# Optimization experiments

Hardware: AMD Instinct MI355X
Metric: run time of the kernel (lower is better)

## Reference

```python
import jax, jax.numpy as jnp
import numpy as np

KS = 3          # kernel_size
NUM_FA = 16     # number of functional atoms per pixel
TOTAL_BASES = 6 # num_bases * (ks // 2)
BN_EPS = 1e-5


def _conv3x3(x, w, b):
    # NCHW conv, padding=1, stride=1
    y = jax.lax.conv_general_dilated(
        x, w, window_strides=(1, 1), padding=[(1, 1), (1, 1)],
        dimension_numbers=("NCHW", "OIHW", "NCHW"))
    return y + b[None, :, None, None]


def _bn(x, gamma, beta, mean, var):
    scale = gamma / jnp.sqrt(var + BN_EPS)
    return (x - mean[None, :, None, None]) * scale[None, :, None, None] + beta[None, :, None, None]


def setup_inputs() -> dict:
    key = jax.random.key(0)
    ks = jax.random.split(key, 16)
    N, C, H, W = 16, 64, 64, 64
    INTER, BC_DIM, O = 64, TOTAL_BASES * NUM_FA, 128
    f32 = jnp.float32
    return {
        "x": jax.random.normal(ks[0], (N, C, H, W), f32),
        "conv1_w": jax.random.normal(ks[1], (INTER, C, 3, 3), f32) * 0.05,
        "conv1_b": jax.random.normal(ks[2], (INTER,), f32) * 0.05,
        "bn1_gamma": jax.random.uniform(ks[3], (INTER,), f32, 0.5, 1.5),
        "bn1_beta": jax.random.normal(ks[4], (INTER,), f32) * 0.05,
        "bn1_mean": jax.random.normal(ks[5], (INTER,), f32) * 0.05,
        "bn1_var": jax.random.uniform(ks[6], (INTER,), f32, 0.5, 1.5),
        "conv2_w": jax.random.normal(ks[7], (BC_DIM, INTER, 3, 3), f32) * 0.05,
        "conv2_b": jax.random.normal(ks[8], (BC_DIM,), f32) * 0.05,
        "bn2_gamma": jax.random.uniform(ks[9], (BC_DIM,), f32, 0.5, 1.5),
        "bn2_beta": jax.random.normal(ks[10], (BC_DIM,), f32) * 0.05,
        "bn2_mean": jax.random.normal(ks[11], (BC_DIM,), f32) * 0.05,
        "bn2_var": jax.random.uniform(ks[12], (BC_DIM,), f32, 0.5, 1.5),
        "bases": jax.random.normal(ks[13], (TOTAL_BASES, KS * KS), f32),
        "coef": jax.random.normal(ks[14], (O, C * NUM_FA), f32) * 0.02,
    }


def reference(x, conv1_w, conv1_b, bn1_gamma, bn1_beta, bn1_mean, bn1_var,
              conv2_w, conv2_b, bn2_gamma, bn2_beta, bn2_mean, bn2_var,
              bases, coef):
    N, C, H, W = x.shape
    # bases_net: conv3x3 -> BN -> tanh -> conv3x3 -> BN -> tanh
    h = jnp.tanh(_bn(_conv3x3(x, conv1_w, conv1_b), bn1_gamma, bn1_beta, bn1_mean, bn1_var))
    bc = jnp.tanh(_bn(_conv3x3(h, conv2_w, conv2_b), bn2_gamma, bn2_beta, bn2_mean, bn2_var))
    # torch: .transpose(1,-1).view(N,H,W,num_fa,total_bases)  (swaps H/W; H==W)
    bases_coef = jnp.transpose(bc, (0, 3, 2, 1)).reshape(N, H, W, NUM_FA, TOTAL_BASES)
    # atoms: (bases_coef[...,None] * bases).sum(-2).transpose(-1,-2) -> (N,H,W,ks2,num_fa)
    atoms = jnp.einsum("nhwft,tk->nhwkf", bases_coef, bases)
    # unfold(x, ks, padding=1) -> patches (N,H,W,C,ks2), channel-major like torch unfold
    xp = jnp.pad(x, ((0, 0), (0, 0), (1, 1), (1, 1)))
    patches = jnp.stack([xp[:, :, i:i + H, j:j + W] for i in range(KS) for j in range(KS)], axis=2)  # (N,C,9,H,W)
    patches = jnp.transpose(patches, (0, 3, 4, 1, 2))  # (N,H,W,C,9)
    # (x.unsqueeze(-1) * atoms.unsqueeze(-3)).sum(-2) -> (N,H,W,C,num_fa) -> flatten C-major
    bases_out = jnp.einsum("nhwck,nhwkf->nhwcf", patches, atoms).reshape(N, H, W, C * NUM_FA)
    # torch: .transpose(1,-1) -> (N, C*num_fa, W, H), then 1x1 conv with coef
    out = jnp.einsum("nhwd,od->nowh", bases_out, coef)  # (N, O, W, H)
    return out
```

## Files before the change

kernel.cpp:

```cpp
#include <hip/hip_runtime.h>
#include <math.h>
#include <string.h>

#define NBATCH 16

typedef __attribute__((ext_vector_type(8))) short short8;
typedef __attribute__((ext_vector_type(4))) float floatx4;
typedef __fp16 half2v __attribute__((ext_vector_type(2)));
#define MFMA16(a, b, c) __builtin_amdgcn_mfma_f32_16x16x32_bf16(a, b, c, 0, 0, 0)

__device__ __forceinline__ unsigned int cvtpk(float a, float b) {
  unsigned int r;
  asm("v_cvt_pk_bf16_f32 %0, %1, %2" : "=v"(r) : "v"(a), "v"(b));
  return r;
}
__device__ __forceinline__ unsigned short f2bf(float f) {
  return (unsigned short)(cvtpk(f, 0.f) & 0xffffu);
}
__device__ __forceinline__ unsigned int packbf2(float a, float b) {
  return cvtpk(a, b);
}
__device__ __forceinline__ float bflo(unsigned int u) {
  return __uint_as_float(u << 16);
}
__device__ __forceinline__ float bfhi(unsigned int u) {
  return __uint_as_float(u & 0xffff0000u);
}
__device__ __forceinline__ float fast_tanh(float x) {
  float e = __expf(2.f * x);
  return 1.f - 2.f / (e + 1.f);
}

__global__ void prep_weights(const float* __restrict__ w1,
                             const float* __restrict__ w2,
                             const float* __restrict__ coef,
                             unsigned short* __restrict__ w1swz,
                             unsigned short* __restrict__ w2swz,
                             unsigned short* __restrict__ coefswz) {
  int i = blockIdx.x * 256 + threadIdx.x;
  if (i < 131072) {
    int j = i & 7, f = i >> 3;
    int lane = f & 63;
    int u = (f >> 6) & 3;
    int wj = (f >> 8) & 1;
    int kc = (f >> 9) & 1;
    int rd = f >> 10;
    int lm = lane & 15, lq = lane >> 4;
    int oc = wj * 64 + u * 16 + lm;
    int k = rd * 64 + kc * 32 + lq * 8 + j;
    coefswz[i] = f2bf(coef[oc * 1024 + k]);
  }
  if (i < 36864) {
    int j = i & 7, f = i >> 3;
    int lane = f & 63;
    int u = (f >> 6) & 1;
    int wn = (f >> 7) & 1;
    int kc = (f >> 8) & 1;
    int off = f >> 9;
    int lm = lane & 15, lq = lane >> 4;
    int oc = wn * 32 + u * 16 + lm;
    int ic = kc * 32 + lq * 8 + j;
    w1swz[i] = f2bf(w1[(oc * 64 + ic) * 9 + off]);
  }
  if (i < 55296) {
    int j = i & 7, f = i >> 3;
    int lane = f & 63;
    int rem = f >> 6;
    int u = rem % 3;
    int rem2 = rem / 3;
    int wn = rem2 & 1;
    int kc = (rem2 >> 1) & 1;
    int off = rem2 >> 2;
    int lm = lane & 15, lq = lane >> 4;
    int oc = wn * 48 + u * 16 + lm;
    int ic = kc * 32 + lq * 8 + j;
    w2swz[i] = f2bf(w2[(oc * 64 + ic) * 9 + off]);
  }
}

__global__ __launch_bounds__(256) void xb_prep(const float* __restrict__ x,
                                               unsigned short* __restrict__ xb) {
  __shared__ float tile[64][65];
  const int t = threadIdx.x;
  const int y = blockIdx.x, n = blockIdx.y;
  const float* xn = x + (size_t)n * 64 * 4096 + y * 64;
#pragma unroll
  for (int it = 0; it < 16; ++it) {
    int idx = it * 256 + t;
    int c = idx >> 6, xx = idx & 63;
    tile[c][xx] = xn[c * 4096 + xx];
  }
  __syncthreads();
  const int xx = t >> 2, cq = t & 3;
  unsigned short* dst = xb + ((size_t)n * 4096 + y * 64 + xx) * 64;
#pragma unroll
  for (int jj = 0; jj < 2; ++jj) {
    int ch0 = cq * 16 + jj * 8;
    unsigned int p[4];
#pragma unroll
    for (int e = 0; e < 4; ++e)
      p[e] = packbf2(tile[ch0 + e * 2][xx], tile[ch0 + e * 2 + 1][xx]);
    *(uint4*)&dst[ch0] = make_uint4(p[0], p[1], p[2], p[3]);
  }
}

__global__ __launch_bounds__(256) void fused_conv(
    const unsigned short* __restrict__ xb, const unsigned short* __restrict__ w1swz,
    const unsigned short* __restrict__ w2swz, const float* __restrict__ b1,
    const float* __restrict__ g1, const float* __restrict__ be1,
    const float* __restrict__ m1, const float* __restrict__ v1,
    const float* __restrict__ b2, const float* __restrict__ g2,
    const float* __restrict__ be2, const float* __restrict__ m2,
    const float* __restrict__ v2, unsigned short* __restrict__ bcg) {
  __shared__ unsigned short xls[144 * 72];
  __shared__ unsigned short hls[128 * 72];

  const int t = threadIdx.x;
  const int tile = blockIdx.x, n = blockIdx.y;
  const int x0 = (tile & 7) * 8, y0 = (tile >> 3) * 8;

  const unsigned short* xbn = xb + (size_t)n * 4096 * 64;
#pragma unroll
  for (int it = 0; it < 5; ++it) {
    int idx = it * 256 + t;
    if (idx < 1152) {
      int pos = idx >> 3, u4 = idx & 7;
      int xr = pos / 12, xc = pos - xr * 12;
      int gy = y0 - 2 + xr, gx = x0 - 2 + xc;
      uint4 v = {0u, 0u, 0u, 0u};
      if ((unsigned)gy < 64u && (unsigned)gx < 64u)
        v = *(const uint4*)&xbn[((size_t)gy * 64 + gx) * 64 + u4 * 8];
      *(uint4*)&xls[pos * 72 + u4 * 8] = v;
    }
  }
  __syncthreads();

  const int lane = t & 63, w = t >> 6;
  const int wm = w & 1, wn = w >> 1;
  const int lm = lane & 15, lq = lane >> 4;

  int abase[4];
#pragma unroll
  for (int i = 0; i < 4; ++i) {
    int px = (wm + 2 * i) * 16 + lm;
    if (px > 99) px = 99;
    int hr = px / 10, hc = px - hr * 10;
    abase[i] = (hr * 12 + hc) * 72 + lq * 8;
  }
  floatx4 acc[4][2];
#pragma unroll
  for (int i = 0; i < 4; ++i)
#pragma unroll
    for (int u = 0; u < 2; ++u) acc[i][u] = floatx4{0.f, 0.f, 0.f, 0.f};

#pragma unroll
  for (int step = 0; step < 18; ++step) {
    const int off = step >> 1, kc = step & 1;
    const int di = off / 3, dj = off % 3;
    short8 b[2];
#pragma unroll
    for (int u = 0; u < 2; ++u)
      b[u] = *(const short8*)&w1swz[(off * 512 + kc * 256 + wn * 128 + u * 64 +
                                     lane) * 8];
#pragma unroll
    for (int i = 0; i < 4; ++i) {
      short8 a = *(const short8*)&xls[abase[i] + (di * 12 + dj) * 72 + kc * 32];
      acc[i][0] = MFMA16(a, b[0], acc[i][0]);
      acc[i][1] = MFMA16(a, b[1], acc[i][1]);
    }
  }
  {
    float sc[2], sh[2];
#pragma unroll
    for (int u = 0; u < 2; ++u) {
      int oc = wn * 32 + u * 16 + lm;
      sc[u] = g1[oc] * rsqrtf(v1[oc] + 1e-5f);
      sh[u] = (b1[oc] - m1[oc]) * sc[u] + be1[oc];
    }
#pragma unroll
    for (int i = 0; i < 4; ++i) {
      int px0 = (wm + 2 * i) * 16 + lq * 4;
#pragma unroll
      for (int u = 0; u < 2; ++u) {
        int oc = wn * 32 + u * 16 + lm;
#pragma unroll
        for (int r = 0; r < 4; ++r) {
          int px = px0 + r;
          if (px < 100) {
            int hr = px / 10, hc = px - hr * 10;
            int gy = y0 - 1 + hr, gx = x0 - 1 + hc;
            bool valid = ((unsigned)gy < 64u) && ((unsigned)gx < 64u);
            float val = valid ? fast_tanh(acc[i][u][r] * sc[u] + sh[u]) : 0.f;
            hls[px * 72 + oc] = f2bf(val);
          }
        }
      }
    }
  }
  __syncthreads();

  int hbase[2];
#pragma unroll
  for (int s = 0; s < 2; ++s) {
    int opx = (wm + 2 * s) * 16 + lm;
    int yl = opx >> 3, xl = opx & 7;
    hbase[s] = (yl * 10 + xl) * 72 + lq * 8;
  }
  floatx4 acc2[2][3];
#pragma unroll
  for (int s = 0; s < 2; ++s)
#pragma unroll
    for (int u = 0; u < 3; ++u) acc2[s][u] = floatx4{0.f, 0.f, 0.f, 0.f};

#pragma unroll
  for (int step = 0; step < 18; ++step) {
    const int off = step >> 1, kc = step & 1;
    const int di = off / 3, dj = off % 3;
    short8 b[3];
#pragma unroll
    for (int u = 0; u < 3; ++u)
      b[u] = *(const short8*)&w2swz[(off * 768 + kc * 384 + wn * 192 + u * 64 +
                                     lane) * 8];
#pragma unroll
    for (int s = 0; s < 2; ++s) {
      short8 a = *(const short8*)&hls[hbase[s] + (di * 10 + dj) * 72 + kc * 32];
      acc2[s][0] = MFMA16(a, b[0], acc2[s][0]);
      acc2[s][1] = MFMA16(a, b[1], acc2[s][1]);
      acc2[s][2] = MFMA16(a, b[2], acc2[s][2]);
    }
  }
  {
    float sc[3], sh[3];
#pragma unroll
    for (int u = 0; u < 3; ++u) {
      int oc = wn * 48 + u * 16 + lm;
      sc[u] = g2[oc] * rsqrtf(v2[oc] + 1e-5f);
      sh[u] = (b2[oc] - m2[oc]) * sc[u] + be2[oc];
    }
    unsigned short* bcn = bcg + (size_t)n * 4096 * 96;
#pragma unroll
    for (int s = 0; s < 2; ++s) {
      int opx0 = (wm + 2 * s) * 16 + lq * 4;
#pragma unroll
      for (int u = 0; u < 3; ++u) {
        int oc = wn * 48 + u * 16 + lm;
#pragma unroll
        for (int r = 0; r < 4; ++r) {
          int opx = opx0 + r;
          int y = y0 + (opx >> 3), xx = x0 + (opx & 7);
          bcn[((size_t)y * 64 + xx) * 96 + oc] =
              f2bf(fast_tanh(acc2[s][u][r] * sc[u] + sh[u]));
        }
      }
    }
  }
}

__global__ __launch_bounds__(256, 2) void adconv_final(
    const unsigned short* __restrict__ xb, const unsigned short* __restrict__ bc,
    const float* __restrict__ bases, const unsigned short* __restrict__ coefswz,
    float* __restrict__ out) {
  __shared__ unsigned short xs[180 * 72];
  __shared__ unsigned short As[4 * 4096];

  const int t = threadIdx.x;
  const int tile = blockIdx.x, n = blockIdx.y;
  const int q0 = (tile & 3) * 16, p0 = (tile >> 2) * 8;

  float bs[54];
#pragma unroll
  for (int i = 0; i < 54; ++i) bs[i] = bases[i];

  const unsigned short* xbn = xb + (size_t)n * 4096 * 64;
#pragma unroll
  for (int it = 0; it < 6; ++it) {
    int idx = it * 256 + t;
    if (idx < 1440) {
      int pos = idx >> 3, u4 = idx & 7;
      int row = pos / 18, col = pos - row * 18;
      int gp = p0 - 1 + row, gq = q0 - 1 + col;
      uint4 v = {0u, 0u, 0u, 0u};
      if ((unsigned)gp < 64u && (unsigned)gq < 64u)
        v = *(const uint4*)&xbn[((size_t)gp * 64 + gq) * 64 + u4 * 8];
      *(uint4*)&xs[pos * 72 + u4 * 8] = v;
    }
  }

  const int lane = t & 63, w = t >> 6;
  const int lm = lane & 15, lq = lane >> 4;

  const int px_a = t >> 1, fh = t & 1;
  const int qx_a = px_a >> 3, py_a = px_a & 7;
  const int pxl_b = lane >> 1;

  half2v atp[9][4];
  {
    const unsigned short* bp =
        bc + ((size_t)n * 4096 + (q0 + qx_a) * 64 + (p0 + py_a)) * 96 + fh * 48;
    float bcv[48];
#pragma unroll
    for (int m = 0; m < 6; ++m) {
      uint4 v = *(const uint4*)(bp + m * 8);
      unsigned int uu[4] = {v.x, v.y, v.z, v.w};
#pragma unroll
      for (int e = 0; e < 4; ++e) {
        bcv[m * 8 + e * 2] = bflo(uu[e]);
        bcv[m * 8 + e * 2 + 1] = bfhi(uu[e]);
      }
    }
#pragma unroll
    for (int j2 = 0; j2 < 4; ++j2)
#pragma unroll
      for (int k = 0; k < 9; ++k) {
        float s0 = 0.f, s1 = 0.f;
#pragma unroll
        for (int tt = 0; tt < 6; ++tt) {
          s0 = fmaf(bcv[(2 * j2) * 6 + tt], bs[tt * 9 + k], s0);
          s1 = fmaf(bcv[(2 * j2 + 1) * 6 + tt], bs[tt * 9 + k], s1);
        }
        atp[k][j2] = __builtin_amdgcn_cvt_pkrtz(s0, s1);
      }
  }

  int pa[9];
#pragma unroll
  for (int i = 0; i < 3; ++i)
#pragma unroll
    for (int j = 0; j < 3; ++j)
      pa[i * 3 + j] = ((py_a + i) * 18 + qx_a + j) * 72;

  floatx4 acc[2][2][4];
#pragma unroll
  for (int s = 0; s < 2; ++s)
#pragma unroll
    for (int wj = 0; wj < 2; ++wj)
#pragma unroll
      for (int u = 0; u < 4; ++u) acc[s][wj][u] = floatx4{0.f, 0.f, 0.f, 0.f};

  unsigned short* Asw = &As[w * 4096];

  uint2 qv[9];
  auto qload = [&](int rd) {
    const int coff = rd * 4;
#pragma unroll
    for (int p = 0; p < 9; ++p) qv[p] = *(const uint2*)&xs[pa[p] + coff];
  };
  auto build = [&](int buf) {
    float a[4][8];
    {
      float c0 = bflo(qv[0].x), c1 = bfhi(qv[0].x);
      float c2 = bflo(qv[0].y), c3 = bfhi(qv[0].y);
#pragma unroll
      for (int j2 = 0; j2 < 4; ++j2) {
        float a0 = (float)atp[0][j2].x, a1 = (float)atp[0][j2].y;
        a[0][2 * j2] = c0 * a0;
        a[0][2 * j2 + 1] = c0 * a1;
        a[1][2 * j2] = c1 * a0;
        a[1][2 * j2 + 1] = c1 * a1;
        a[2][2 * j2] = c2 * a0;
        a[2][2 * j2 + 1] = c2 * a1;
        a[3][2 * j2] = c3 * a0;
        a[3][2 * j2 + 1] = c3 * a1;
      }
    }
#pragma unroll
    for (int p = 1; p < 9; ++p) {
      float c0 = bflo(qv[p].x), c1 = bfhi(qv[p].x);
      float c2 = bflo(qv[p].y), c3 = bfhi(qv[p].y);
#pragma unroll
      for (int j2 = 0; j2 < 4; ++j2) {
        float a0 = (float)atp[p][j2].x, a1 = (float)atp[p][j2].y;
        a[0][2 * j2] = fmaf(c0, a0, a[0][2 * j2]);
        a[0][2 * j2 + 1] = fmaf(c0, a1, a[0][2 * j2 + 1]);
        a[1][2 * j2] = fmaf(c1, a0, a[1][2 * j2]);
        a[1][2 * j2 + 1] = fmaf(c1, a1, a[1][2 * j2 + 1]);
        a[2][2 * j2] = fmaf(c2, a0, a[2][2 * j2]);
        a[2][2 * j2 + 1] = fmaf(c2, a1, a[2][2 * j2 + 1]);
        a[3][2 * j2] = fmaf(c3, a0, a[3][2 * j2]);
        a[3][2 * j2 + 1] = fmaf(c3, a1, a[3][2 * j2 + 1]);
      }
    }
    unsigned short* dstw = Asw + buf * 2048;
#pragma unroll
    for (int cc = 0; cc < 4; ++cc) {
      int g = pxl_b * 8 + ((cc * 2 + fh) ^ (pxl_b & 7));
      *(uint4*)&dstw[g * 8] =
          make_uint4(cvtpk(a[cc][0], a[cc][1]), cvtpk(a[cc][2], a[cc][3]),
                     cvtpk(a[cc][4], a[cc][5]), cvtpk(a[cc][6], a[cc][7]));
    }
  };

  __syncthreads();
  qload(0);
  build(0);

  for (int rd = 0; rd < 16; ++rd) {
    const int buf = rd & 1;
    if (rd < 15) qload(rd + 1);
    short8 Af[2][2];
#pragma unroll
    for (int s = 0; s < 2; ++s) {
      int pxl = s * 16 + lm;
#pragma unroll
      for (int kc = 0; kc < 2; ++kc) {
        int g = pxl * 8 + ((kc * 4 + lq) ^ (pxl & 7));
        Af[s][kc] = *(const short8*)&Asw[buf * 2048 + g * 8];
      }
    }
    short8 Bf0[2][4];
#pragma unroll
    for (int wj = 0; wj < 2; ++wj)
#pragma unroll
      for (int u = 0; u < 4; ++u) {
        int frag = ((rd * 2 + 0) * 2 + wj) * 4 + u;
        Bf0[wj][u] = *(const short8*)(coefswz + ((size_t)frag * 64 + lane) * 8);
      }
    if (rd < 15) build(buf ^ 1);
    short8 Bf1[2][4];
#pragma unroll
    for (int wj = 0; wj < 2; ++wj)
#pragma unroll
      for (int u = 0; u < 4; ++u) {
        int frag = ((rd * 2 + 1) * 2 + wj) * 4 + u;
        Bf1[wj][u] = *(const short8*)(coefswz + ((size_t)frag * 64 + lane) * 8);
      }
    __builtin_amdgcn_s_setprio(1);
#pragma unroll
    for (int wj = 0; wj < 2; ++wj)
#pragma unroll
      for (int u = 0; u < 4; ++u)
#pragma unroll
        for (int s = 0; s < 2; ++s)
          acc[s][wj][u] = MFMA16(Af[s][0], Bf0[wj][u], acc[s][wj][u]);
#pragma unroll
    for (int wj = 0; wj < 2; ++wj)
#pragma unroll
      for (int u = 0; u < 4; ++u)
#pragma unroll
        for (int s = 0; s < 2; ++s)
          acc[s][wj][u] = MFMA16(Af[s][1], Bf1[wj][u], acc[s][wj][u]);
    __builtin_amdgcn_s_setprio(0);
  }

  float* outn = out + (size_t)n * 128 * 4096;
#pragma unroll
  for (int wj = 0; wj < 2; ++wj)
#pragma unroll
    for (int u = 0; u < 4; ++u) {
      int oc = wj * 64 + u * 16 + lm;
#pragma unroll
      for (int s = 0; s < 2; ++s) {
        int px0 = w * 32 + s * 16 + lq * 4;
        int qx = px0 >> 3, py0 = px0 & 7;
        *(float4*)&outn[((size_t)oc * 64 + q0 + qx) * 64 + p0 + py0] =
            make_float4(acc[s][wj][u][0], acc[s][wj][u][1], acc[s][wj][u][2],
                        acc[s][wj][u][3]);
      }
    }
}

extern "C" void kernel_launch(void* const* d_in, const int* in_sizes, int n_in,
                              void* d_out, int out_size, void* d_ws,
                              size_t ws_size, hipStream_t stream) {
  const float* x = (const float*)d_in[0];
  const float* conv1_w = (const float*)d_in[1];
  const float* conv1_b = (const float*)d_in[2];
  const float* bn1_g = (const float*)d_in[3];
  const float* bn1_b = (const float*)d_in[4];
  const float* bn1_m = (const float*)d_in[5];
  const float* bn1_v = (const float*)d_in[6];
  const float* conv2_w = (const float*)d_in[7];
  const float* conv2_b = (const float*)d_in[8];
  const float* bn2_g = (const float*)d_in[9];
  const float* bn2_b = (const float*)d_in[10];
  const float* bn2_m = (const float*)d_in[11];
  const float* bn2_v = (const float*)d_in[12];
  const float* bases = (const float*)d_in[13];
  const float* coef = (const float*)d_in[14];
  float* out = (float*)d_out;

  char* ws = (char*)d_ws;
  unsigned short* xbuf = (unsigned short*)(ws);
  unsigned short* bcb = (unsigned short*)(ws + 8388608);
  unsigned short* w1swz = (unsigned short*)(ws + 20971520);
  unsigned short* w2swz = (unsigned short*)(ws + 21045248);
  unsigned short* coefswz = (unsigned short*)(ws + 21155840);

  prep_weights<<<512, 256, 0, stream>>>(conv1_w, conv2_w, coef, w1swz, w2swz,
                                        coefswz);
  xb_prep<<<dim3(64, NBATCH), 256, 0, stream>>>(x, xbuf);
  fused_conv<<<dim3(64, NBATCH), 256, 0, stream>>>(
      xbuf, w1swz, w2swz, conv1_b, bn1_g, bn1_b, bn1_m, bn1_v, conv2_b, bn2_g,
      bn2_b, bn2_m, bn2_v, bcb);
  adconv_final<<<dim3(32, NBATCH), 256, 0, stream>>>(xbuf, bcb, bases, coefswz,
                                                     out);
}
```

Measured before the change: 167.3 us.

## Shrink adconv_final tile to 8x8 pixels and raise occupancy

Each adconv_final block now covers an 8x8 pixel tile instead of 16x8. Each wave handles 16 pixels, and each thread builds 4 functional-atom features rather than 8. The A staging buffer drops from double to single buffering, which shrinks LDS and register use so three blocks per CU can fit, and the grid doubles to improve parallelism. In exchange, the halo overhead per tile grows and each block reloads the full coefficient matrix, so coefficient traffic from L2 doubles.

```diff
diff --git a/kernel.cpp b/kernel.cpp
--- a/kernel.cpp
+++ b/kernel.cpp
@@ -256,16 +256,16 @@
   }
 }
 
-__global__ __launch_bounds__(256, 2) void adconv_final(
+__global__ __launch_bounds__(256, 3) void adconv_final(
     const unsigned short* __restrict__ xb, const unsigned short* __restrict__ bc,
     const float* __restrict__ bases, const unsigned short* __restrict__ coefswz,
     float* __restrict__ out) {
-  __shared__ unsigned short xs[180 * 72];
-  __shared__ unsigned short As[4 * 4096];
+  __shared__ unsigned short xs[100 * 72];
+  __shared__ unsigned short As[4 * 1024];
 
   const int t = threadIdx.x;
   const int tile = blockIdx.x, n = blockIdx.y;
-  const int q0 = (tile & 3) * 16, p0 = (tile >> 2) * 8;
+  const int q0 = (tile & 7) * 8, p0 = (tile >> 3) * 8;
 
   float bs[54];
 #pragma unroll
@@ -273,11 +273,11 @@
 
   const unsigned short* xbn = xb + (size_t)n * 4096 * 64;
 #pragma unroll
-  for (int it = 0; it < 6; ++it) {
+  for (int it = 0; it < 4; ++it) {
     int idx = it * 256 + t;
-    if (idx < 1440) {
+    if (idx < 800) {
       int pos = idx >> 3, u4 = idx & 7;
-      int row = pos / 18, col = pos - row * 18;
+      int row = pos / 10, col = pos - row * 10;
       int gp = p0 - 1 + row, gq = q0 - 1 + col;
       uint4 v = {0u, 0u, 0u, 0u};
       if ((unsigned)gp < 64u && (unsigned)gq < 64u)
@@ -289,17 +289,17 @@
   const int lane = t & 63, w = t >> 6;
   const int lm = lane & 15, lq = lane >> 4;
 
-  const int px_a = t >> 1, fh = t & 1;
-  const int qx_a = px_a >> 3, py_a = px_a & 7;
-  const int pxl_b = lane >> 1;
-
-  half2v atp[9][4];
+  const int pxl_b = lane >> 2, fh4 = lane & 3;
+  const int px_b = w * 16 + pxl_b;
+  const int qx_b = px_b >> 3, py_b = px_b & 7;
+
+  half2v atp[9][2];
   {
     const unsigned short* bp =
-        bc + ((size_t)n * 4096 + (q0 + qx_a) * 64 + (p0 + py_a)) * 96 + fh * 48;
-    float bcv[48];
-#pragma unroll
-    for (int m = 0; m < 6; ++m) {
+        bc + ((size_t)n * 4096 + (q0 + qx_b) * 64 + (p0 + py_b)) * 96 + fh4 * 24;
+    float bcv[24];
+#pragma unroll
+    for (int m = 0; m < 3; ++m) {
       uint4 v = *(const uint4*)(bp + m * 8);
       unsigned int uu[4] = {v.x, v.y, v.z, v.w};
 #pragma unroll
@@ -309,7 +309,7 @@
       }
     }
 #pragma unroll
-    for (int j2 = 0; j2 < 4; ++j2)
+    for (int j2 = 0; j2 < 2; ++j2)
 #pragma unroll
       for (int k = 0; k < 9; ++k) {
         float s0 = 0.f, s1 = 0.f;
@@ -327,17 +327,15 @@
   for (int i = 0; i < 3; ++i)
 #pragma unroll
     for (int j = 0; j < 3; ++j)
-      pa[i * 3 + j] = ((py_a + i) * 18 + qx_a + j) * 72;
-
-  floatx4 acc[2][2][4];
-#pragma unroll
-  for (int s = 0; s < 2; ++s)
-#pragma unroll
-    for (int wj = 0; wj < 2; ++wj)
-#pragma unroll
-      for (int u = 0; u < 4; ++u) acc[s][wj][u] = floatx4{0.f, 0.f, 0.f, 0.f};
-
-  unsigned short* Asw = &As[w * 4096];
+      pa[i * 3 + j] = ((py_b + i) * 10 + qx_b + j) * 72;
+
+  floatx4 acc[2][4];
+#pragma unroll
+  for (int wj = 0; wj < 2; ++wj)
+#pragma unroll
+    for (int u = 0; u < 4; ++u) acc[wj][u] = floatx4{0.f, 0.f, 0.f, 0.f};
+
+  unsigned short* Asw = &As[w * 1024];
 
   uint2 qv[9];
   auto qload = [&](int rd) {
@@ -345,13 +343,13 @@
 #pragma unroll
     for (int p = 0; p < 9; ++p) qv[p] = *(const uint2*)&xs[pa[p] + coff];
   };
-  auto build = [&](int buf) {
-    float a[4][8];
+  auto build = [&]() {
+    float a[4][4];
     {
       float c0 = bflo(qv[0].x), c1 = bfhi(qv[0].x);
       float c2 = bflo(qv[0].y), c3 = bfhi(qv[0].y);
 #pragma unroll
-      for (int j2 = 0; j2 < 4; ++j2) {
+      for (int j2 = 0; j2 < 2; ++j2) {
         float a0 = (float)atp[0][j2].x, a1 = (float)atp[0][j2].y;
         a[0][2 * j2] = c0 * a0;
         a[0][2 * j2 + 1] = c0 * a1;
@@ -368,7 +366,7 @@
       float c0 = bflo(qv[p].x), c1 = bfhi(qv[p].x);
       float c2 = bflo(qv[p].y), c3 = bfhi(qv[p].y);
 #pragma unroll
-      for (int j2 = 0; j2 < 4; ++j2) {
+      for (int j2 = 0; j2 < 2; ++j2) {
         float a0 = (float)atp[p][j2].x, a1 = (float)atp[p][j2].y;
         a[0][2 * j2] = fmaf(c0, a0, a[0][2 * j2]);
         a[0][2 * j2 + 1] = fmaf(c0, a1, a[0][2 * j2 + 1]);
@@ -380,66 +378,65 @@
         a[3][2 * j2 + 1] = fmaf(c3, a1, a[3][2 * j2 + 1]);
       }
     }
-    unsigned short* dstw = Asw + buf * 2048;
 #pragma unroll
     for (int cc = 0; cc < 4; ++cc) {
-      int g = pxl_b * 8 + ((cc * 2 + fh) ^ (pxl_b & 7));
-      *(uint4*)&dstw[g * 8] =
-          make_uint4(cvtpk(a[cc][0], a[cc][1]), cvtpk(a[cc][2], a[cc][3]),
-                     cvtpk(a[cc][4], a[cc][5]), cvtpk(a[cc][6], a[cc][7]));
+      int g = (cc * 4 + fh4) ^ ((pxl_b & 7) << 1);
+      uint2 val;
+      val.x = cvtpk(a[cc][0], a[cc][1]);
+      val.y = cvtpk(a[cc][2], a[cc][3]);
+      *(uint2*)&Asw[pxl_b * 64 + g * 4] = val;
     }
   };
 
   __syncthreads();
   qload(0);
-  build(0);
+  build();
 
   for (int rd = 0; rd < 16; ++rd) {
-    const int buf = rd & 1;
-    if (rd < 15) qload(rd + 1);
-    short8 Af[2][2];
-#pragma unroll
-    for (int s = 0; s < 2; ++s) {
-      int pxl = s * 16 + lm;
-#pragma unroll
-      for (int kc = 0; kc < 2; ++kc) {
-        int g = pxl * 8 + ((kc * 4 + lq) ^ (pxl & 7));
-        Af[s][kc] = *(const short8*)&Asw[buf * 2048 + g * 8];
-      }
-    }
-    short8 Bf0[2][4];
-#pragma unroll
-    for (int wj = 0; wj < 2; ++wj)
-#pragma unroll
-      for (int u = 0; u < 4; ++u) {
-        int frag = ((rd * 2 + 0) * 2 + wj) * 4 + u;
-        Bf0[wj][u] = *(const short8*)(coefswz + ((size_t)frag * 64 + lane) * 8);
-      }
-    if (rd < 15) build(buf ^ 1);
-    short8 Bf1[2][4];
-#pragma unroll
-    for (int wj = 0; wj < 2; ++wj)
-#pragma unroll
-      for (int u = 0; u < 4; ++u) {
-        int frag = ((rd * 2 + 1) * 2 + wj) * 4 + u;
-        Bf1[wj][u] = *(const short8*)(coefswz + ((size_t)frag * 64 + lane) * 8);
-      }
-    __builtin_amdgcn_s_setprio(1);
-#pragma unroll
-    for (int wj = 0; wj < 2; ++wj)
-#pragma unroll
-      for (int u = 0; u < 4; ++u)
-#pragma unroll
-        for (int s = 0; s < 2; ++s)
-          acc[s][wj][u] = MFMA16(Af[s][0], Bf0[wj][u], acc[s][wj][u]);
-#pragma unroll
-    for (int wj = 0; wj < 2; ++wj)
-#pragma unroll
-      for (int u = 0; u < 4; ++u)
-#pragma unroll
-        for (int s = 0; s < 2; ++s)
-          acc[s][wj][u] = MFMA16(Af[s][1], Bf1[wj][u], acc[s][wj][u]);
-    __builtin_amdgcn_s_setprio(0);
+    short8 Af[2];
+#pragma unroll
+    for (int kc = 0; kc < 2; ++kc) {
+      int u16 = (kc * 4 + lq) ^ (lm & 7);
+      Af[kc] = *(const short8*)&Asw[lm * 64 + u16 * 8];
+    }
+    if (rd < 15) {
+      qload(rd + 1);
+      build();
+    }
+    {
+      short8 Bf[2][4];
+#pragma unroll
+      for (int wj = 0; wj < 2; ++wj)
+#pragma unroll
+        for (int u = 0; u < 4; ++u) {
+          int frag = ((rd * 2 + 0) * 2 + wj) * 4 + u;
+          Bf[wj][u] = *(const short8*)(coefswz + ((size_t)frag * 64 + lane) * 8);
+        }
+      __builtin_amdgcn_s_setprio(1);
+#pragma unroll
+      for (int wj = 0; wj < 2; ++wj)
+#pragma unroll
+        for (int u = 0; u < 4; ++u)
+          acc[wj][u] = MFMA16(Af[0], Bf[wj][u], acc[wj][u]);
+      __builtin_amdgcn_s_setprio(0);
+    }
+    {
+      short8 Bf[2][4];
+#pragma unroll
+      for (int wj = 0; wj < 2; ++wj)
+#pragma unroll
+        for (int u = 0; u < 4; ++u) {
+          int frag = ((rd * 2 + 1) * 2 + wj) * 4 + u;
+          Bf[wj][u] = *(const short8*)(coefswz + ((size_t)frag * 64 + lane) * 8);
+        }
+      __builtin_amdgcn_s_setprio(1);
+#pragma unroll
+      for (int wj = 0; wj < 2; ++wj)
+#pragma unroll
+        for (int u = 0; u < 4; ++u)
+          acc[wj][u] = MFMA16(Af[1], Bf[wj][u], acc[wj][u]);
+      __builtin_amdgcn_s_setprio(0);
+    }
   }
 
   float* outn = out + (size_t)n * 128 * 4096;
@@ -448,14 +445,11 @@
 #pragma unroll
     for (int u = 0; u < 4; ++u) {
       int oc = wj * 64 + u * 16 + lm;
-#pragma unroll
-      for (int s = 0; s < 2; ++s) {
-        int px0 = w * 32 + s * 16 + lq * 4;
-        int qx = px0 >> 3, py0 = px0 & 7;
-        *(float4*)&outn[((size_t)oc * 64 + q0 + qx) * 64 + p0 + py0] =
-            make_float4(acc[s][wj][u][0], acc[s][wj][u][1], acc[s][wj][u][2],
-                        acc[s][wj][u][3]);
-      }
+      int gpx = w * 16 + lq * 4;
+      int qx = gpx >> 3, py0 = gpx & 7;
+      *(float4*)&outn[((size_t)oc * 64 + q0 + qx) * 64 + p0 + py0] =
+          make_float4(acc[wj][u][0], acc[wj][u][1], acc[wj][u][2],
+                      acc[wj][u][3]);
     }
 }
 
@@ -492,6 +486,6 @@
   fused_conv<<<dim3(64, NBATCH), 256, 0, stream>>>(
       xbuf, w1swz, w2swz, conv1_b, bn1_g, bn1_b, bn1_m, bn1_v, conv2_b, bn2_g,
       bn2_b, bn2_m, bn2_v, bcb);
-  adconv_final<<<dim3(32, NBATCH), 256, 0, stream>>>(xbuf, bcb, bases, coefswz,
+  adconv_final<<<dim3(64, NBATCH), 256, 0, stream>>>(xbuf, bcb, bases, coefswz,
                                                      out);
 }
```

Result: no change. 169.1 us (+1.0%).
